# Kernel optimization log

Hardware: AMD Instinct MI355X
Metric: run time of the kernel (lower is better)

Reference implementation:

```python
import jax, jax.numpy as jnp
import numpy as np
from jax import lax

POOL_SIZES = (1, 3, 5, 7, 14)  # PyramidSample bins -> 1+9+25+49+196 = 280 positions


def _pool_mat(in_size, out_size):
    # exact torch adaptive_avg_pool1d bin boundaries as a [out, in] averaging matrix
    P = np.zeros((out_size, in_size), np.float32)
    for i in range(out_size):
        s = (i * in_size) // out_size
        e = -((-(i + 1) * in_size) // out_size)
        P[i, s:e] = 1.0 / (e - s)
    return jnp.asarray(P)


def _psp(x):
    # x: [B, C, H, W] -> [B, C, 280]
    B, C, H, W = x.shape
    outs = []
    for s in POOL_SIZES:
        Ph, Pw = _pool_mat(H, s), _pool_mat(W, s)
        y = jnp.einsum('oh,bchw,pw->bcop', Ph, x, Pw)  # adaptive avg pool to [s,s]
        outs.append(y.reshape(B, C, s * s))
    return jnp.concatenate(outs, axis=-1)


def setup_inputs() -> dict:
    key = jax.random.key(0)
    ks = jax.random.split(key, 7)
    B, C, H, W = 8, 256, 96, 96
    c8 = max(4, C // 8)  # 32
    return {
        'x_1': jax.random.normal(ks[0], (B, C, H, W), jnp.float32),
        'x':   jax.random.normal(ks[1], (B, C, H, W), jnp.float32),
        'wq':  jax.random.normal(ks[2], (C, C), jnp.float32) * 0.05,
        'bq':  jax.random.normal(ks[3], (C,), jnp.float32) * 0.05,
        'wk':  jax.random.normal(ks[4], (c8, C), jnp.float32) * 0.05,
        'bk':  jax.random.normal(ks[5], (c8,), jnp.float32) * 0.05,
        'con': jax.random.normal(ks[6], (c8, C, 3, 3), jnp.float32),
    }


def reference(x_1, x, wq, bq, wk, bk, con):
    B, C, H, W = x.shape
    c8 = wk.shape[0]
    # 1x1 convs
    q = jnp.einsum('oc,bchw->bohw', wq, x_1) + bq[None, :, None, None]
    k = jnp.einsum('oc,bchw->bohw', wk, x) + bk[None, :, None, None]
    proj_query = _psp(q)                         # [B, C, 280]
    proj_key = _psp(k)                           # [B, c8, 280]
    aff = jax.nn.sigmoid(jnp.einsum('bcp,bkp->bck', proj_query, proj_key))  # [B, C, c8]
    # synthesize per-sample dynamic 3x3 weights: [B*C, C, 3, 3]
    agg_w = (aff.reshape(B * C, c8) @ con.reshape(c8, C * 9)).reshape(B * C, C, 3, 3)
    # grouped conv, groups = B
    xg = x_1.reshape(1, B * C, H, W)
    out = lax.conv_general_dilated(
        xg, agg_w, window_strides=(1, 1), padding=((1, 1), (1, 1)),
        dimension_numbers=('NCHW', 'OIHW', 'NCHW'), feature_group_count=B)
    return out.reshape(B, C, H, W)
```

## Files before the change

### kernel.cpp

```cpp
#include <hip/hip_runtime.h>
#include <hip/hip_bf16.h>


#define B 8
#define C 256
#define C8 32
#define H 96
#define W 96
#define HW 9216
#define NPOS 280
#define NWBIN 30
#define RPS 108
#define OTS 68
#define XCH 260
#define PKS 284

typedef __attribute__((ext_vector_type(8))) short short8;
typedef __attribute__((ext_vector_type(4))) float float4v;
typedef __attribute__((ext_vector_type(4))) unsigned short ushort4v;

static __device__ __forceinline__ unsigned short f2bf(float f) {
    unsigned u = __float_as_uint(f);
    unsigned r = (u + 0x7FFF + ((u >> 16) & 1)) >> 16;
    return (unsigned short)r;
}
static __device__ __forceinline__ float bf2f(unsigned short h) {
    unsigned u = ((unsigned)h) << 16;
    return __uint_as_float(u);
}

template<int H0>
static __device__ __forceinline__ void accum_half_col(const float* __restrict__ col0,
                                                      float acc[NWBIN]) {
    const int SC[5]   = {1, 3, 5, 7, 14};
    const int WOFF[5] = {0, 1, 4, 9, 16};
    #pragma unroll
    for (int k = 0; k < NWBIN; ++k) acc[k] = 0.f;
    #pragma unroll
    for (int g = 0; g < 4; ++g) {
        float v[12];
        #pragma unroll
        for (int q = 0; q < 12; ++q) v[q] = col0[(size_t)(H0 + g * 12 + q) * 96];
        #pragma unroll
        for (int q = 0; q < 12; ++q) {
            const int h = H0 + g * 12 + q;
            #pragma unroll
            for (int si = 0; si < 5; ++si) {
                #pragma unroll
                for (int j = 0; j < SC[si]; ++j) {
                    const int st = (j * 96) / SC[si];
                    const int en = (96 * (j + 1) + SC[si] - 1) / SC[si];
                    if (h >= st && h < en) acc[WOFF[si] + j] += v[q];
                }
            }
        }
    }
}

__global__ __launch_bounds__(256) void pool_kernel(const float* __restrict__ x1,
                                                   const float* __restrict__ x,
                                                   float* __restrict__ px1,
                                                   float* __restrict__ px) {
    __shared__ __align__(16) float colp[NWBIN * RPS];
    const int bi = blockIdx.x;
    const int which = bi >> 11;
    const int bc = bi & 2047;
    const float* __restrict__ src = (which ? x : x1) + (size_t)bc * HW;
    float* __restrict__ dst = (which ? px : px1) + (size_t)bc * NPOS;
    const int tid = threadIdx.x;

    const int SC[5]   = {1, 3, 5, 7, 14};
    const int WOFF[5] = {0, 1, 4, 9, 16};
    const int POFF[5] = {0, 1, 10, 35, 84};

    float acc[NWBIN];
    if (tid < 96) {
        accum_half_col<0>(src + tid, acc);
    } else if (tid >= 128 && tid < 224) {
        accum_half_col<48>(src + (tid - 128), acc);
    }

    if (tid >= 128 && tid < 224) {
        const int w1 = tid - 128;
        #pragma unroll
        for (int si = 0; si < 5; ++si) {
            #pragma unroll
            for (int i = 0; i < SC[si]; ++i)
                colp[(WOFF[si] + i) * RPS + w1] = acc[WOFF[si] + i];
        }
    }
    __syncthreads();
    if (tid < 96) {
        #pragma unroll
        for (int si = 0; si < 5; ++si) {
            #pragma unroll
            for (int i = 0; i < SC[si]; ++i) {
                const int st = (i * 96) / SC[si];
                const int en = (96 * (i + 1) + SC[si] - 1) / SC[si];
                const float inv = 1.0f / (float)(en - st);
                const int bin = WOFF[si] + i;
                colp[bin * RPS + tid] = (acc[bin] + colp[bin * RPS + tid]) * inv;
            }
        }
    }
    __syncthreads();

    if (tid < NWBIN) {
        float run = 0.f;
        #pragma unroll
        for (int c = 0; c < 24; ++c) {
            float4 v = *(const float4*)&colp[tid * RPS + 4 * c];
            v.x += run; v.y += v.x; v.z += v.y; v.w += v.z;
            run = v.w;
            *(float4*)&colp[tid * RPS + 4 * c] = v;
        }
    }
    __syncthreads();

    for (int p = tid; p < NPOS; p += 256) {
        int si;
        if (p < 1) si = 0; else if (p < 10) si = 1; else if (p < 35) si = 2;
        else if (p < 84) si = 3; else si = 4;
        int s = SC[si];
        int loc = p - POFF[si];
        int i = loc / s;
        int j = loc - i * s;
        int st = (j * 96) / s;
        int en = (96 * (j + 1) + s - 1) / s;
        int binrow = WOFF[si] + i;
        float hi = colp[binrow * RPS + (en - 1)];
        float lo = (st > 0) ? colp[binrow * RPS + (st - 1)] : 0.f;
        dst[p] = (hi - lo) * (1.0f / (float)(en - st));
    }
}

__global__ __launch_bounds__(320) void proj_kernel(const float* __restrict__ px1,
                                                   const float* __restrict__ px,
                                                   const float* __restrict__ wq,
                                                   const float* __restrict__ bq,
                                                   const float* __restrict__ wk,
                                                   const float* __restrict__ bk,
                                                   float* __restrict__ PQ,
                                                   float* __restrict__ PK) {
    __shared__ float wt[16 * 256];
    const int bi = blockIdx.x;
    const int b = bi / 18;
    const int r = bi % 18;
    const int tid = threadIdx.x;
    const float* src;
    const float* wm;
    const float* bias;
    float* dst;
    int o0;
    if (r < 16) {
        o0 = r * 16;
        src = px1 + (size_t)b * C * NPOS;
        wm = wq; bias = bq;
        dst = PQ + ((size_t)b * C + o0) * NPOS;
    } else {
        o0 = (r - 16) * 16;
        src = px + (size_t)b * C * NPOS;
        wm = wk; bias = bk;
        dst = PK + ((size_t)b * C8 + o0) * NPOS;
    }
    for (int idx = tid; idx < 4096; idx += 320) wt[idx] = wm[o0 * C + idx];
    __syncthreads();
    if (tid >= NPOS) return;

    float acc[16];
    #pragma unroll
    for (int i = 0; i < 16; ++i) acc[i] = 0.f;
    #pragma unroll 4
    for (int c = 0; c < C; ++c) {
        float xv = src[c * NPOS + tid];
        #pragma unroll
        for (int i = 0; i < 16; ++i)
            acc[i] += wt[i * 256 + c] * xv;
    }
    #pragma unroll
    for (int i = 0; i < 16; ++i)
        dst[i * NPOS + tid] = acc[i] + bias[o0 + i];
}

__global__ __launch_bounds__(256) void aff_kernel(const float* __restrict__ PQ,
                                                  const float* __restrict__ PK,
                                                  unsigned short* __restrict__ affb) {
    __shared__ __align__(16) float pk[C8 * PKS];
    const int bi = blockIdx.x;
    const int b = bi >> 5;
    const int og = bi & 31;
    const int tid = threadIdx.x;

    const float* __restrict__ pkb = PK + (size_t)b * C8 * NPOS;
    for (int idx = tid; idx < 2240; idx += 256) {
        int row = idx / 70;
        int c4 = idx - row * 70;
        *(float4*)&pk[row * PKS + c4 * 4] = *(const float4*)&pkb[row * NPOS + c4 * 4];
    }
    __syncthreads();

    const int k = tid & 31;
    const int o = og * 8 + (tid >> 5);
    const float4* __restrict__ q4 = (const float4*)(PQ + ((size_t)b * C + o) * NPOS);
    const float4* __restrict__ p4 = (const float4*)&pk[k * PKS];
    float acc = 0.f;
    #pragma unroll 10
    for (int i = 0; i < NPOS / 4; ++i) {
        float4 a = q4[i];
        float4 c = p4[i];
        acc += a.x * c.x + a.y * c.y + a.z * c.z + a.w * c.w;
    }
    float s = 1.0f / (1.0f + __expf(-acc));
    affb[((size_t)b * C + o) * C8 + k] = f2bf(s);
}

__global__ __launch_bounds__(256) void aswz_kernel(const float* __restrict__ con,
                                                   unsigned short* __restrict__ aswz) {
    int idx = blockIdx.x * 256 + threadIdx.x;
    if (idx >= 73728) return;
    int j = idx & 7;
    int lane = (idx >> 3) & 63;
    int mt = (idx >> 9) & 1;
    int s = idx >> 10;
    int pos = s >> 3;
    int cg = s & 7;
    int m = lane & 15, quad = lane >> 4;
    int ko = mt * 16 + m;
    int c = cg * 32 + quad * 8 + j;
    int dy = pos / 3, dx = pos - dy * 3;
    float v = con[((ko * C + c) * 3 + dy) * 3 + dx];
    aswz[idx] = f2bf(v);
}

__global__ __launch_bounds__(256) void x2bf_kernel(const float* __restrict__ x1,
                                                   unsigned short* __restrict__ xbf) {
    __shared__ __align__(16) unsigned short tl[64 * XCH];
    const int bi = blockIdx.x;
    const int b = bi / 144;
    const int pt = bi % 144;
    const int p0 = pt * 64;
    const int wid = threadIdx.x >> 6;
    const int lane = threadIdx.x & 63;

    #pragma unroll 8
    for (int it = 0; it < 64; ++it) {
        int ch = it * 4 + wid;
        float v = x1[((size_t)(b * C + ch)) * HW + p0 + lane];
        tl[lane * XCH + ch] = f2bf(v);
    }
    __syncthreads();
    #pragma unroll
    for (int it = 0; it < 16; ++it) {
        int pr = it * 4 + wid;
        ushort4v v = *(const ushort4v*)&tl[pr * XCH + lane * 4];
        *(ushort4v*)&xbf[((size_t)b * HW + p0 + pr) * 256 + lane * 4] = v;
    }
}

__global__ __launch_bounds__(256) void yconv_mfma(const unsigned short* __restrict__ xbf,
                                                  const unsigned short* __restrict__ aswz,
                                                  unsigned short* __restrict__ Yp) {
    __shared__ unsigned short xsl[10 * 50 * 40];
    const int bi = blockIdx.x;
    const int kc = bi & 3;
    const int rest = bi >> 2;
    const int tilex = rest & 1;
    const int tiley = (rest >> 1) % 12;
    const int b = rest / 24;
    const int tid = threadIdx.x;
    const int wid = tid >> 6;
    const int lane = tid & 63;
    const int n = lane & 15, quad = lane >> 4;

    float4v acc[2][6];
    #pragma unroll
    for (int mt = 0; mt < 2; ++mt)
        #pragma unroll
        for (int t = 0; t < 6; ++t)
            acc[mt][t] = (float4v){0.f, 0.f, 0.f, 0.f};

    int baseb[6];
    #pragma unroll
    for (int t = 0; t < 6; ++t) {
        int tt = wid * 6 + t;
        int rt = tt / 3;
        int xb = (tt % 3) * 16;
        baseb[t] = (rt * 50 + xb + n) * 40 + quad * 8;
    }

    for (int ci = 0; ci < 2; ++ci) {
        const int cg = kc * 2 + ci;
        __syncthreads();
        for (int task = tid; task < 2000; task += 256) {
            int pix = task >> 2;
            int cq = task & 3;
            int r = pix / 50;
            int col = pix - r * 50;
            int gy = tiley * 8 + r - 1;
            int gx = tilex * 48 + col - 1;
            uint4 v = make_uint4(0u, 0u, 0u, 0u);
            if ((unsigned)gy < 96u && (unsigned)gx < 96u)
                v = *(const uint4*)&xbf[((size_t)b * HW + gy * 96 + gx) * 256 + cg * 32 + cq * 8];
            *(uint4*)&xsl[(r * 50 + col) * 40 + cq * 8] = v;
        }
        short8 af[9][2];
        #pragma unroll
        for (int pos = 0; pos < 9; ++pos)
            #pragma unroll
            for (int mt = 0; mt < 2; ++mt)
                af[pos][mt] = *(const short8*)&aswz[((((pos * 8 + cg) * 2) + mt) * 64 + lane) * 8];
        __syncthreads();

        #pragma unroll
        for (int pos = 0; pos < 9; ++pos) {
            const int dy = pos / 3, dx = pos - (pos / 3) * 3;
            const int d = (dy * 50 + dx) * 40;
            #pragma unroll
            for (int t = 0; t < 6; ++t) {
                short8 bf = *(const short8*)&xsl[baseb[t] + d];
                acc[0][t] = __builtin_amdgcn_mfma_f32_16x16x32_bf16(af[pos][0], bf, acc[0][t], 0, 0, 0);
                acc[1][t] = __builtin_amdgcn_mfma_f32_16x16x32_bf16(af[pos][1], bf, acc[1][t], 0, 0, 0);
            }
        }
    }

    #pragma unroll
    for (int mt = 0; mt < 2; ++mt) {
        #pragma unroll
        for (int t = 0; t < 6; ++t) {
            int tt = wid * 6 + t;
            int rt = tt / 3;
            int xb = (tt % 3) * 16;
            int gy = tiley * 8 + rt;
            int gx = tilex * 48 + xb + n;
            ushort4v v;
            #pragma unroll
            for (int reg = 0; reg < 4; ++reg) v[reg] = f2bf(acc[mt][t][reg]);
            *(ushort4v*)&Yp[((((size_t)kc * B + b) * HW + gy * 96 + gx)) * C8 + mt * 16 + quad * 4] = v;
        }
    }
}

__global__ __launch_bounds__(256) void mix_kernel(const unsigned short* __restrict__ Yp,
                                                  const unsigned short* __restrict__ affb,
                                                  float* __restrict__ out) {
    __shared__ float ot[128 * OTS];
    const int bi = blockIdx.x;
    const int b = bi / 144;
    const int pg = bi % 144;
    const int wid = threadIdx.x >> 6;
    const int lane = threadIdx.x & 63;
    const int n = lane & 15, quad = lane >> 4;
    const int px0 = pg * 64 + wid * 16;

    short8 y0 = *(const short8*)&Yp[(((size_t)0 * B + b) * HW + px0 + n) * C8 + quad * 8];
    short8 y1 = *(const short8*)&Yp[(((size_t)1 * B + b) * HW + px0 + n) * C8 + quad * 8];
    short8 y2 = *(const short8*)&Yp[(((size_t)2 * B + b) * HW + px0 + n) * C8 + quad * 8];
    short8 y3 = *(const short8*)&Yp[(((size_t)3 * B + b) * HW + px0 + n) * C8 + quad * 8];

    float4v acc[16];
    #pragma unroll
    for (int mt = 0; mt < 16; ++mt) acc[mt] = (float4v){0.f, 0.f, 0.f, 0.f};

    #pragma unroll
    for (int mt = 0; mt < 16; ++mt) {
        const short8 a = *(const short8*)&affb[((size_t)b * C + mt * 16 + n) * C8 + quad * 8];
        acc[mt] = __builtin_amdgcn_mfma_f32_16x16x32_bf16(a, y0, acc[mt], 0, 0, 0);
        acc[mt] = __builtin_amdgcn_mfma_f32_16x16x32_bf16(a, y1, acc[mt], 0, 0, 0);
        acc[mt] = __builtin_amdgcn_mfma_f32_16x16x32_bf16(a, y2, acc[mt], 0, 0, 0);
        acc[mt] = __builtin_amdgcn_mfma_f32_16x16x32_bf16(a, y3, acc[mt], 0, 0, 0);
    }

    #pragma unroll
    for (int half = 0; half < 2; ++half) {
        __syncthreads();
        #pragma unroll
        for (int mt = 0; mt < 8; ++mt) {
            #pragma unroll
            for (int reg = 0; reg < 4; ++reg) {
                ot[(mt * 16 + quad * 4 + reg) * OTS + wid * 16 + n] = acc[half * 8 + mt][reg];
            }
        }
        __syncthreads();
        #pragma unroll
        for (int i = 0; i < 32; ++i) {
            int o = wid * 32 + i;
            out[((size_t)b * C + half * 128 + o) * HW + pg * 64 + lane] = ot[o * OTS + lane];
        }
    }
}

extern "C" void kernel_launch(void* const* d_in, const int* in_sizes, int n_in,
                              void* d_out, int out_size, void* d_ws, size_t ws_size,
                              hipStream_t stream) {
    const float* x1  = (const float*)d_in[0];
    const float* x   = (const float*)d_in[1];
    const float* wq  = (const float*)d_in[2];
    const float* bq  = (const float*)d_in[3];
    const float* wk  = (const float*)d_in[4];
    const float* bk  = (const float*)d_in[5];
    const float* con = (const float*)d_in[6];
    float* out = (float*)d_out;

    float* ws = (float*)d_ws;
    unsigned short* affb = (unsigned short*)ws;
    unsigned short* aswz = (unsigned short*)(ws + 65536);
    float* px1 = ws + 102400;
    float* px  = ws + 675840;
    float* PQ  = ws + 1249280;
    float* PK  = ws + 1822720;
    unsigned short* xbf = (unsigned short*)(ws + 102400);
    unsigned short* Yp  = (unsigned short*)(ws + 9539584);

    aswz_kernel<<<288, 256, 0, stream>>>(con, aswz);
    pool_kernel<<<4096, 256, 0, stream>>>(x1, x, px1, px);
    proj_kernel<<<B * 18, 320, 0, stream>>>(px1, px, wq, bq, wk, bk, PQ, PK);
    aff_kernel<<<B * 32, 256, 0, stream>>>(PQ, PK, affb);
    x2bf_kernel<<<1152, 256, 0, stream>>>(x1, xbf);
    yconv_mfma<<<768, 256, 0, stream>>>(xbf, aswz, Yp);
    mix_kernel<<<1152, 256, 0, stream>>>(Yp, affb, out);
}
```

Measured before the change: 293.2 us.

## Move projection and affinity GEMMs to bf16 MFMA with transposed pooled layout

The pooling kernel now writes its pooled features as bf16, transposed to position-major [B, 288, C] and zero-padded from 280 to 288 positions. The 1x1 projection and the affinity dot products, previously scalar fp32 FMA loops, become bf16 MFMA 16x16x32 kernels, and the projection outputs are stored as padded bf16 rows. This aims to cut the small but serial cost of the proj and aff stages and to halve their intermediate traffic. The trade-off is less precision in the affinity path, plus strided 2-byte scattered stores in pool_kernel.

```diff
diff --git a/kernel.cpp b/kernel.cpp
--- a/kernel.cpp
+++ b/kernel.cpp
@@ -9,11 +9,12 @@
 #define W 96
 #define HW 9216
 #define NPOS 280
+#define NP 288
 #define NWBIN 30
 #define RPS 108
 #define OTS 68
 #define XCH 260
-#define PKS 284
+#define PJS 304
 
 typedef __attribute__((ext_vector_type(8))) short short8;
 typedef __attribute__((ext_vector_type(4))) float float4v;
@@ -59,14 +60,16 @@
 
 __global__ __launch_bounds__(256) void pool_kernel(const float* __restrict__ x1,
                                                    const float* __restrict__ x,
-                                                   float* __restrict__ px1,
-                                                   float* __restrict__ px) {
+                                                   unsigned short* __restrict__ px1t,
+                                                   unsigned short* __restrict__ pxt) {
     __shared__ __align__(16) float colp[NWBIN * RPS];
     const int bi = blockIdx.x;
     const int which = bi >> 11;
     const int bc = bi & 2047;
     const float* __restrict__ src = (which ? x : x1) + (size_t)bc * HW;
-    float* __restrict__ dst = (which ? px : px1) + (size_t)bc * NPOS;
+    const int b = bc >> 8;
+    const int c = bc & 255;
+    unsigned short* __restrict__ dstT = (which ? pxt : px1t) + ((size_t)b * NP) * C + c;
     const int tid = threadIdx.x;
 
     const int SC[5]   = {1, 3, 5, 7, 14};
@@ -108,11 +111,11 @@
     if (tid < NWBIN) {
         float run = 0.f;
         #pragma unroll
-        for (int c = 0; c < 24; ++c) {
-            float4 v = *(const float4*)&colp[tid * RPS + 4 * c];
+        for (int cc = 0; cc < 24; ++cc) {
+            float4 v = *(const float4*)&colp[tid * RPS + 4 * cc];
             v.x += run; v.y += v.x; v.z += v.y; v.w += v.z;
             run = v.w;
-            *(float4*)&colp[tid * RPS + 4 * c] = v;
+            *(float4*)&colp[tid * RPS + 4 * cc] = v;
         }
     }
     __syncthreads();
@@ -130,88 +133,118 @@
         int binrow = WOFF[si] + i;
         float hi = colp[binrow * RPS + (en - 1)];
         float lo = (st > 0) ? colp[binrow * RPS + (st - 1)] : 0.f;
-        dst[p] = (hi - lo) * (1.0f / (float)(en - st));
-    }
-}
-
-__global__ __launch_bounds__(320) void proj_kernel(const float* __restrict__ px1,
-                                                   const float* __restrict__ px,
-                                                   const float* __restrict__ wq,
-                                                   const float* __restrict__ bq,
-                                                   const float* __restrict__ wk,
-                                                   const float* __restrict__ bk,
-                                                   float* __restrict__ PQ,
-                                                   float* __restrict__ PK) {
-    __shared__ float wt[16 * 256];
+        dstT[(size_t)p * C] = f2bf((hi - lo) * (1.0f / (float)(en - st)));
+    }
+    if (tid < NP - NPOS) dstT[(size_t)(NPOS + tid) * C] = 0;
+}
+
+__global__ __launch_bounds__(256) void proj_mfma(const unsigned short* __restrict__ px1t,
+                                                 const unsigned short* __restrict__ pxt,
+                                                 const float* __restrict__ wq,
+                                                 const float* __restrict__ bq,
+                                                 const float* __restrict__ wk,
+                                                 const float* __restrict__ bk,
+                                                 unsigned short* __restrict__ PQb,
+                                                 unsigned short* __restrict__ PKb) {
+    __shared__ __align__(16) unsigned short lds[16 * PJS];
     const int bi = blockIdx.x;
     const int b = bi / 18;
-    const int r = bi % 18;
+    const int mt = bi % 18;
     const int tid = threadIdx.x;
-    const float* src;
-    const float* wm;
-    const float* bias;
-    float* dst;
-    int o0;
-    if (r < 16) {
-        o0 = r * 16;
-        src = px1 + (size_t)b * C * NPOS;
-        wm = wq; bias = bq;
-        dst = PQ + ((size_t)b * C + o0) * NPOS;
-    } else {
-        o0 = (r - 16) * 16;
-        src = px + (size_t)b * C * NPOS;
-        wm = wk; bias = bk;
-        dst = PK + ((size_t)b * C8 + o0) * NPOS;
-    }
-    for (int idx = tid; idx < 4096; idx += 320) wt[idx] = wm[o0 * C + idx];
+    const int wid = tid >> 6;
+    const int lane = tid & 63;
+    const int n = lane & 15, quad = lane >> 4;
+    const bool isQ = (mt < 16);
+    const int row0 = isQ ? mt * 16 : (mt - 16) * 16;
+    const float* __restrict__ wm = isQ ? wq : wk;
+    const float* __restrict__ bias = isQ ? bq : bk;
+    const unsigned short* __restrict__ src = (isQ ? px1t : pxt) + (size_t)b * NP * C;
+
+    short8 af[8];
+    #pragma unroll
+    for (int ks = 0; ks < 8; ++ks) {
+        const float* wr = &wm[(row0 + n) * C + ks * 32 + quad * 8];
+        short8 a;
+        #pragma unroll
+        for (int j = 0; j < 8; ++j) a[j] = (short)f2bf(wr[j]);
+        af[ks] = a;
+    }
+
+    float4v acc[5];
+    #pragma unroll
+    for (int t = 0; t < 5; ++t) acc[t] = (float4v){0.f, 0.f, 0.f, 0.f};
+
+    #pragma unroll
+    for (int t = 0; t < 5; ++t) {
+        const int nt = t * 4 + wid;
+        if (nt < 18) {
+            #pragma unroll
+            for (int ks = 0; ks < 8; ++ks) {
+                short8 bf = *(const short8*)&src[(size_t)(nt * 16 + n) * C + ks * 32 + quad * 8];
+                acc[t] = __builtin_amdgcn_mfma_f32_16x16x32_bf16(af[ks], bf, acc[t], 0, 0, 0);
+            }
+        }
+    }
+
+    #pragma unroll
+    for (int t = 0; t < 5; ++t) {
+        const int nt = t * 4 + wid;
+        if (nt < 18) {
+            #pragma unroll
+            for (int reg = 0; reg < 4; ++reg) {
+                float v = acc[t][reg] + bias[row0 + quad * 4 + reg];
+                lds[(quad * 4 + reg) * PJS + nt * 16 + n] = f2bf(v);
+            }
+        }
+    }
     __syncthreads();
-    if (tid >= NPOS) return;
-
-    float acc[16];
-    #pragma unroll
-    for (int i = 0; i < 16; ++i) acc[i] = 0.f;
-    #pragma unroll 4
-    for (int c = 0; c < C; ++c) {
-        float xv = src[c * NPOS + tid];
-        #pragma unroll
-        for (int i = 0; i < 16; ++i)
-            acc[i] += wt[i * 256 + c] * xv;
-    }
-    #pragma unroll
-    for (int i = 0; i < 16; ++i)
-        dst[i * NPOS + tid] = acc[i] + bias[o0 + i];
-}
-
-__global__ __launch_bounds__(256) void aff_kernel(const float* __restrict__ PQ,
-                                                  const float* __restrict__ PK,
-                                                  unsigned short* __restrict__ affb) {
-    __shared__ __align__(16) float pk[C8 * PKS];
-    const int bi = blockIdx.x;
-    const int b = bi >> 5;
-    const int og = bi & 31;
+    unsigned short* __restrict__ dstb = isQ ? PQb + ((size_t)b * C + row0) * NP
+                                            : PKb + ((size_t)b * C8 + row0) * NP;
+    for (int idx = tid; idx < 16 * 144; idx += 256) {
+        int r = idx / 144;
+        int c2 = idx - r * 144;
+        unsigned int v = 0u;
+        if (c2 < 140) v = *(const unsigned int*)&lds[r * PJS + c2 * 2];
+        ((unsigned int*)&dstb[(size_t)r * NP])[c2] = v;
+    }
+}
+
+__global__ __launch_bounds__(256) void aff_mfma(const unsigned short* __restrict__ PQb,
+                                                const unsigned short* __restrict__ PKb,
+                                                unsigned short* __restrict__ affb) {
+    const int bi = blockIdx.x;
+    const int b = bi >> 2;
+    const int og = bi & 3;
     const int tid = threadIdx.x;
-
-    const float* __restrict__ pkb = PK + (size_t)b * C8 * NPOS;
-    for (int idx = tid; idx < 2240; idx += 256) {
-        int row = idx / 70;
-        int c4 = idx - row * 70;
-        *(float4*)&pk[row * PKS + c4 * 4] = *(const float4*)&pkb[row * NPOS + c4 * 4];
-    }
-    __syncthreads();
-
-    const int k = tid & 31;
-    const int o = og * 8 + (tid >> 5);
-    const float4* __restrict__ q4 = (const float4*)(PQ + ((size_t)b * C + o) * NPOS);
-    const float4* __restrict__ p4 = (const float4*)&pk[k * PKS];
-    float acc = 0.f;
-    #pragma unroll 10
-    for (int i = 0; i < NPOS / 4; ++i) {
-        float4 a = q4[i];
-        float4 c = p4[i];
-        acc += a.x * c.x + a.y * c.y + a.z * c.z + a.w * c.w;
-    }
-    float s = 1.0f / (1.0f + __expf(-acc));
-    affb[((size_t)b * C + o) * C8 + k] = f2bf(s);
+    const int wid = tid >> 6;
+    const int lane = tid & 63;
+    const int n = lane & 15, quad = lane >> 4;
+    const int o = og * 64 + wid * 16 + n;
+
+    float4v acc[2];
+    acc[0] = (float4v){0.f, 0.f, 0.f, 0.f};
+    acc[1] = (float4v){0.f, 0.f, 0.f, 0.f};
+
+    #pragma unroll
+    for (int ks = 0; ks < 9; ++ks) {
+        short8 bfr = *(const short8*)&PQb[((size_t)b * C + o) * NP + ks * 32 + quad * 8];
+        #pragma unroll
+        for (int mt = 0; mt < 2; ++mt) {
+            short8 a = *(const short8*)&PKb[((size_t)b * C8 + mt * 16 + n) * NP + ks * 32 + quad * 8];
+            acc[mt] = __builtin_amdgcn_mfma_f32_16x16x32_bf16(a, bfr, acc[mt], 0, 0, 0);
+        }
+    }
+
+    #pragma unroll
+    for (int mt = 0; mt < 2; ++mt) {
+        ushort4v v;
+        #pragma unroll
+        for (int reg = 0; reg < 4; ++reg) {
+            float s = 1.0f / (1.0f + __expf(-acc[mt][reg]));
+            v[reg] = f2bf(s);
+        }
+        *(ushort4v*)&affb[((size_t)b * C + o) * C8 + mt * 16 + quad * 4] = v;
+    }
 }
 
 __global__ __launch_bounds__(256) void aswz_kernel(const float* __restrict__ con,
@@ -405,17 +438,17 @@
     float* ws = (float*)d_ws;
     unsigned short* affb = (unsigned short*)ws;
     unsigned short* aswz = (unsigned short*)(ws + 65536);
-    float* px1 = ws + 102400;
-    float* px  = ws + 675840;
-    float* PQ  = ws + 1249280;
-    float* PK  = ws + 1822720;
+    unsigned short* px1t = (unsigned short*)(ws + 102400);
+    unsigned short* pxt  = (unsigned short*)(ws + 397312);
+    unsigned short* PQb  = (unsigned short*)(ws + 692224);
+    unsigned short* PKb  = (unsigned short*)(ws + 987136);
     unsigned short* xbf = (unsigned short*)(ws + 102400);
     unsigned short* Yp  = (unsigned short*)(ws + 9539584);
 
     aswz_kernel<<<288, 256, 0, stream>>>(con, aswz);
-    pool_kernel<<<4096, 256, 0, stream>>>(x1, x, px1, px);
-    proj_kernel<<<B * 18, 320, 0, stream>>>(px1, px, wq, bq, wk, bk, PQ, PK);
-    aff_kernel<<<B * 32, 256, 0, stream>>>(PQ, PK, affb);
+    pool_kernel<<<4096, 256, 0, stream>>>(x1, x, px1t, pxt);
+    proj_mfma<<<B * 18, 256, 0, stream>>>(px1t, pxt, wq, bq, wk, bk, PQb, PKb);
+    aff_mfma<<<B * 4, 256, 0, stream>>>(PQb, PKb, affb);
     x2bf_kernel<<<1152, 256, 0, stream>>>(x1, xbf);
     yconv_mfma<<<768, 256, 0, stream>>>(xbf, aswz, Yp);
     mix_kernel<<<1152, 256, 0, stream>>>(Yp, affb, out);
```

Result: faster. 269.6 us (-8.1%).
